# Kernel tuning notes

Hardware: AMD Instinct MI355X
Metric: run time of the kernel (lower is better)

## Reference

```python
import jax, jax.numpy as jnp
import numpy as np
import math

IN_FEATURES = 1024
OUT_FEATURES = 1024
N_BANK = 8192
N_LAYER = 12
N_EMBD = 1024


def setup_inputs() -> dict:
    key = jax.random.key(0)
    kq, kk, kv = jax.random.split(key, 3)
    q = jax.random.normal(kq, (4, 2048, IN_FEATURES), dtype=jnp.float32)
    k = 0.02 * jax.random.normal(kk, (N_BANK, IN_FEATURES), dtype=jnp.float32)
    v_std = 2.0 / N_LAYER / math.sqrt(N_EMBD)
    v = v_std * jax.random.normal(kv, (N_BANK, OUT_FEATURES), dtype=jnp.float32)
    return {"q": q, "k": k, "v": v}


def reference(q, k, v):
    # scores: [B, T, N]
    scores = jnp.einsum("btd,nd->btn", q, k)
    # row-wise L2 normalization, scaled by sqrt(N), then exact (erf) GELU
    sqrt_n = jnp.sqrt(jnp.asarray(scores.shape[-1], scores.dtype))
    norm = jnp.linalg.norm(scores, axis=-1, keepdims=True)
    gated = jax.nn.gelu(scores / norm * sqrt_n, approximate=False)
    # out: [B, T, out_features]
    return jnp.einsum("btn,no->bto", gated, v)
```

## Files before the change

### kernel.cpp

```cpp
#include <hip/hip_runtime.h>
#include <hip/hip_bf16.h>
#include <math.h>


#define MROWS 8192
#define DIN   1024
#define NBANK 8192
#define DOUT  1024

typedef float  f32x4  __attribute__((ext_vector_type(4)));
typedef __bf16 bf16x8 __attribute__((ext_vector_type(8)));

__device__ __forceinline__ float bf2f(unsigned short u) {
  union { unsigned int i; float f; } x; x.i = ((unsigned int)u) << 16; return x.f;
}
__device__ __forceinline__ unsigned short f2bf(float f) {
  union { float f; unsigned int i; } x; x.f = f;
  unsigned int u = x.i;
  unsigned int r = (u + 0x7fffu + ((u >> 16) & 1u)) >> 16;
  return (unsigned short)r;
}

__global__ void cvt_kernel(const float* __restrict__ src,
                           unsigned short* __restrict__ dst, int n) {
  int i = (blockIdx.x * 256 + threadIdx.x) * 4;
  if (i >= n) return;
  float4 vv = *(const float4*)(src + i);
  ushort4 o;
  o.x = f2bf(vv.x); o.y = f2bf(vv.y); o.z = f2bf(vv.z); o.w = f2bf(vv.w);
  *(ushort4*)(dst + i) = o;
}

__global__ void transpose_cvt_kernel(const float* __restrict__ src,
                                     unsigned short* __restrict__ dst,
                                     int R, int C) {
  __shared__ float tile[32][33];
  int c0 = blockIdx.x * 32, r0 = blockIdx.y * 32;
  for (int i = threadIdx.y; i < 32; i += 8)
    tile[i][threadIdx.x] = src[(size_t)(r0 + i) * C + c0 + threadIdx.x];
  __syncthreads();
  for (int i = threadIdx.y; i < 32; i += 8)
    dst[(size_t)(c0 + i) * R + r0 + threadIdx.x] = f2bf(tile[threadIdx.x][i]);
}

__global__ void zero_f32_kernel(float* __restrict__ p, int n4) {
  int i = blockIdx.x * 256 + threadIdx.x;
  if (i < n4) ((float4*)p)[i] = make_float4(0.f, 0.f, 0.f, 0.f);
}

__global__ __launch_bounds__(512, 4) void gemm1_kernel(
    const unsigned short* __restrict__ A, const unsigned short* __restrict__ B,
    unsigned short* __restrict__ C, float* __restrict__ sumsq) {
  __shared__ unsigned short As[3 * 4096];
  __shared__ unsigned short Bs[3 * 8192];
  const int K = DIN;
  const int NKT = DIN / 32;

  const int tid  = threadIdx.x;
  const int lane = tid & 63;
  const int wm   = (tid >> 6) >> 2;
  const int wn   = (tid >> 6) & 3;
  const int quad = lane >> 4;
  const int l16  = lane & 15;

  const int flat = blockIdx.y * gridDim.x + blockIdx.x;
  const int nwg  = gridDim.x * gridDim.y;
  const int swz  = (flat & 7) * (nwg >> 3) + (flat >> 3);
  const size_t m0 = (size_t)(swz / gridDim.x) * 128;
  const size_t n0 = (size_t)(swz % gridDim.x) * 256;

  const int sw   = (l16 >> 1) & 3;
  const int aoff = (wm * 64 + l16) * 32 + (quad ^ sw) * 8;
  const int boff = (wn * 64 + l16) * 32 + (quad ^ sw) * 8;

  const int gslot = (tid & 3) ^ ((tid >> 3) & 3);
  const unsigned short* Ag = A + (m0 + (tid >> 2)) * (size_t)K + gslot * 8;
  const unsigned short* Bg = B + (n0 + (tid >> 2)) * (size_t)K + gslot * 8;

  f32x4 acc[4][4];
#pragma unroll
  for (int i = 0; i < 4; i++)
#pragma unroll
    for (int j = 0; j < 4; j++) {
      f32x4 z = {0.f, 0.f, 0.f, 0.f};
      acc[i][j] = z;
    }

  auto stage = [&](int buf, int koff) {
    __builtin_amdgcn_global_load_lds(
        (const __attribute__((address_space(1))) unsigned int*)(Ag + koff),
        (__attribute__((address_space(3))) unsigned int*)(As + buf * 4096 + tid * 8),
        16, 0, 0);
    __builtin_amdgcn_global_load_lds(
        (const __attribute__((address_space(1))) unsigned int*)(Bg + koff),
        (__attribute__((address_space(3))) unsigned int*)(Bs + buf * 8192 + tid * 8),
        16, 0, 0);
    __builtin_amdgcn_global_load_lds(
        (const __attribute__((address_space(1))) unsigned int*)(Bg + (size_t)128 * K +
                                                                koff),
        (__attribute__((address_space(3))) unsigned int*)(Bs + buf * 8192 + 4096 +
                                                          tid * 8),
        16, 0, 0);
  };

  stage(0, 0);
  stage(1, 32);
  asm volatile("s_waitcnt vmcnt(3)" ::: "memory");
  __builtin_amdgcn_s_barrier();
  __builtin_amdgcn_sched_barrier(0);

  int cur = 0;
  for (int t = 0; t < NKT; ++t) {
    const bool pf = (t + 2) < NKT;
    if (pf) {
      int nxt = cur + 2;
      if (nxt >= 3) nxt -= 3;
      stage(nxt, (t + 2) * 32);
    }

    const unsigned short* Ab = As + cur * 4096 + aoff;
    const unsigned short* Bb = Bs + cur * 8192 + boff;
    bf16x8 a[4], b[4];
#pragma unroll
    for (int i = 0; i < 4; ++i) a[i] = *(const bf16x8*)(Ab + i * 512);
#pragma unroll
    for (int j = 0; j < 4; ++j) b[j] = *(const bf16x8*)(Bb + j * 512);

    asm volatile("s_waitcnt lgkmcnt(0)" ::: "memory");
    __builtin_amdgcn_sched_barrier(0);
    __builtin_amdgcn_s_setprio(1);
#pragma unroll
    for (int i = 0; i < 4; ++i)
#pragma unroll
      for (int j = 0; j < 4; ++j)
        acc[i][j] = __builtin_amdgcn_mfma_f32_16x16x32_bf16(a[i], b[j], acc[i][j],
                                                            0, 0, 0);
    __builtin_amdgcn_s_setprio(0);

    if (pf)
      asm volatile("s_waitcnt vmcnt(3)" ::: "memory");
    else
      asm volatile("s_waitcnt vmcnt(0)" ::: "memory");
    __builtin_amdgcn_s_barrier();
    __builtin_amdgcn_sched_barrier(0);

    cur = (cur == 2) ? 0 : cur + 1;
  }

#pragma unroll
  for (int mf = 0; mf < 4; ++mf)
#pragma unroll
    for (int r = 0; r < 4; ++r) {
      size_t row = m0 + wm * 64 + mf * 16 + quad * 4 + r;
      float s = 0.f;
#pragma unroll
      for (int nf = 0; nf < 4; ++nf) {
        float val = acc[mf][nf][r];
        s += val * val;
        C[row * (size_t)NBANK + n0 + wn * 64 + nf * 16 + l16] = f2bf(val);
      }
      s += __shfl_xor(s, 1);
      s += __shfl_xor(s, 2);
      s += __shfl_xor(s, 4);
      s += __shfl_xor(s, 8);
      if (l16 == 0) atomicAdd(&sumsq[row], s);
    }
}

__global__ void gelu_kernel(unsigned short* __restrict__ S,
                            const float* __restrict__ sumsq) {
  const size_t total = (size_t)MROWS * NBANK / 8;
  for (size_t u = (size_t)blockIdx.x * 256 + threadIdx.x; u < total;
       u += (size_t)gridDim.x * 256) {
    size_t idx = u * 8;
    int row = (int)(idx >> 13);
    float sc = sqrtf((float)NBANK / sumsq[row]);
    uint4 vv = *(const uint4*)(S + idx);
    unsigned int w[4] = {vv.x, vv.y, vv.z, vv.w};
#pragma unroll
    for (int e = 0; e < 4; e++) {
      float x0 = bf2f((unsigned short)(w[e] & 0xffffu)) * sc;
      float x1 = bf2f((unsigned short)(w[e] >> 16)) * sc;
      float g0 = 0.5f * x0 * (1.0f + erff(x0 * 0.70710678118654752f));
      float g1 = 0.5f * x1 * (1.0f + erff(x1 * 0.70710678118654752f));
      w[e] = (unsigned int)f2bf(g0) | ((unsigned int)f2bf(g1) << 16);
    }
    uint4 o; o.x = w[0]; o.y = w[1]; o.z = w[2]; o.w = w[3];
    *(uint4*)(S + idx) = o;
  }
}

__global__ __launch_bounds__(256, 4) void gemm2_kernel(
    const unsigned short* __restrict__ A,
    const unsigned short* __restrict__ B,
    float* __restrict__ C) {
  __shared__ unsigned short As[128 * 32];
  __shared__ unsigned short Bs[128 * 32];
  const int K = NBANK, ldc = DOUT;

  const int tid  = threadIdx.x;
  const int lane = tid & 63;
  const int wave = tid >> 6;
  const int wm   = (wave >> 1) * 64;
  const int wn   = (wave & 1) * 64;
  const int quad = lane >> 4;
  const int l16  = lane & 15;

  const int flat = blockIdx.y * gridDim.x + blockIdx.x;
  const int nwg  = gridDim.x * gridDim.y;
  const int swz  = (flat & 7) * (nwg >> 3) + (flat >> 3);
  const size_t m0 = (size_t)(swz / gridDim.x) * 128;
  const size_t n0 = (size_t)(swz % gridDim.x) * 128;

  const int srow = tid >> 2;
  const int scol = (((tid & 3) ^ ((tid >> 3) & 3))) * 8;
  const unsigned short* Ag0 = A + (m0 + srow) * (size_t)K + scol;
  const unsigned short* Ag1 = A + (m0 + srow + 64) * (size_t)K + scol;
  const unsigned short* Bg0 = B + (n0 + srow) * (size_t)K + scol;
  const unsigned short* Bg1 = B + (n0 + srow + 64) * (size_t)K + scol;

  unsigned short* AsW0 = As + tid * 8;
  unsigned short* AsW1 = As + 64 * 32 + tid * 8;
  unsigned short* BsW0 = Bs + tid * 8;
  unsigned short* BsW1 = Bs + 64 * 32 + tid * 8;

  const int sw = (l16 >> 1) & 3;
  const unsigned short* ArP = As + (wm + l16) * 32 + (quad ^ sw) * 8;
  const unsigned short* BrP = Bs + (wn + l16) * 32 + (quad ^ sw) * 8;

  f32x4 acc[4][4];
#pragma unroll
  for (int i = 0; i < 4; i++)
#pragma unroll
    for (int j = 0; j < 4; j++) {
      f32x4 z = {0.f, 0.f, 0.f, 0.f};
      acc[i][j] = z;
    }

  for (int k0 = 0; k0 < K; k0 += 32) {
    __builtin_amdgcn_global_load_lds(
        (const __attribute__((address_space(1))) unsigned int*)(Ag0 + k0),
        (__attribute__((address_space(3))) unsigned int*)AsW0, 16, 0, 0);
    __builtin_amdgcn_global_load_lds(
        (const __attribute__((address_space(1))) unsigned int*)(Ag1 + k0),
        (__attribute__((address_space(3))) unsigned int*)AsW1, 16, 0, 0);
    __builtin_amdgcn_global_load_lds(
        (const __attribute__((address_space(1))) unsigned int*)(Bg0 + k0),
        (__attribute__((address_space(3))) unsigned int*)BsW0, 16, 0, 0);
    __builtin_amdgcn_global_load_lds(
        (const __attribute__((address_space(1))) unsigned int*)(Bg1 + k0),
        (__attribute__((address_space(3))) unsigned int*)BsW1, 16, 0, 0);
    __syncthreads();

    bf16x8 af[4], bfr[4];
#pragma unroll
    for (int i = 0; i < 4; i++) af[i] = *(const bf16x8*)(ArP + i * 16 * 32);
#pragma unroll
    for (int j = 0; j < 4; j++) bfr[j] = *(const bf16x8*)(BrP + j * 16 * 32);
#pragma unroll
    for (int i = 0; i < 4; i++)
#pragma unroll
      for (int j = 0; j < 4; j++)
        acc[i][j] = __builtin_amdgcn_mfma_f32_16x16x32_bf16(af[i], bfr[j],
                                                            acc[i][j], 0, 0, 0);
    __syncthreads();
  }

#pragma unroll
  for (int i = 0; i < 4; i++)
#pragma unroll
    for (int j = 0; j < 4; j++)
#pragma unroll
      for (int r = 0; r < 4; r++) {
        size_t row = m0 + wm + i * 16 + quad * 4 + r;
        size_t col = n0 + wn + j * 16 + l16;
        C[row * (size_t)ldc + col] = acc[i][j][r];
      }
}

extern "C" void kernel_launch(void* const* d_in, const int* in_sizes, int n_in,
                              void* d_out, int out_size, void* d_ws, size_t ws_size,
                              hipStream_t stream) {
  const float* q = (const float*)d_in[0];
  const float* k = (const float*)d_in[1];
  const float* v = (const float*)d_in[2];
  float* out = (float*)d_out;

  char* ws = (char*)d_ws;
  const size_t MB = 1024ull * 1024ull;
  unsigned short* qb     = (unsigned short*)(ws);
  unsigned short* kb     = (unsigned short*)(ws + 16 * MB);
  unsigned short* vbT    = (unsigned short*)(ws + 32 * MB);
  unsigned short* scores = (unsigned short*)(ws + 48 * MB);
  float*          scale  = (float*)(ws + 176 * MB);

  const int nqk = MROWS * DIN;

  zero_f32_kernel<<<(MROWS / 4 + 255) / 256, 256, 0, stream>>>(scale, MROWS / 4);

  cvt_kernel<<<nqk / 1024, 256, 0, stream>>>(q, qb, nqk);
  cvt_kernel<<<nqk / 1024, 256, 0, stream>>>(k, kb, nqk);
  transpose_cvt_kernel<<<dim3(DOUT / 32, NBANK / 32), dim3(32, 8), 0, stream>>>(
      v, vbT, NBANK, DOUT);

  gemm1_kernel<<<dim3(NBANK / 256, MROWS / 128), 512, 0, stream>>>(qb, kb, scores,
                                                                   scale);

  gelu_kernel<<<4096, 256, 0, stream>>>(scores, scale);

  gemm2_kernel<<<dim3(DOUT / 128, MROWS / 128), 256, 0, stream>>>(scores, vbT, out);
}
```

Measured before the change: 551.0 us.

## Merge prep kernels, enlarge GEMM1 tile to 256x256, use sigmoid GELU approximation

Folds the zeroing, the two bf16 conversions and the V transpose into one prep kernel launch to cut launch overhead. GEMM1 moves from 128x256 to 256x256 tiles with 8x4 MFMA fragments per wave and drops the 3-stage LDS ring for plain double buffering, raising arithmetic intensity at the cost of more registers and a shallower prefetch. The exact erf GELU is replaced by a tanh-style sigmoid approximation using fast exp and rcp, which cuts transcendental cost but changes the numerics slightly.

New measurement: 1.673 ms. 204% more time.

```diff
diff --git a/kernel.cpp b/kernel.cpp
--- a/kernel.cpp
+++ b/kernel.cpp
@@ -21,38 +21,43 @@
   return (unsigned short)r;
 }
 
-__global__ void cvt_kernel(const float* __restrict__ src,
-                           unsigned short* __restrict__ dst, int n) {
-  int i = (blockIdx.x * 256 + threadIdx.x) * 4;
-  if (i >= n) return;
-  float4 vv = *(const float4*)(src + i);
-  ushort4 o;
-  o.x = f2bf(vv.x); o.y = f2bf(vv.y); o.z = f2bf(vv.z); o.w = f2bf(vv.w);
-  *(ushort4*)(dst + i) = o;
-}
-
-__global__ void transpose_cvt_kernel(const float* __restrict__ src,
-                                     unsigned short* __restrict__ dst,
-                                     int R, int C) {
+__global__ void prep_kernel(const float* __restrict__ q, const float* __restrict__ k,
+                            const float* __restrict__ v,
+                            unsigned short* __restrict__ qb,
+                            unsigned short* __restrict__ kb,
+                            unsigned short* __restrict__ vbT,
+                            float* __restrict__ sumsq) {
   __shared__ float tile[32][33];
-  int c0 = blockIdx.x * 32, r0 = blockIdx.y * 32;
-  for (int i = threadIdx.y; i < 32; i += 8)
-    tile[i][threadIdx.x] = src[(size_t)(r0 + i) * C + c0 + threadIdx.x];
-  __syncthreads();
-  for (int i = threadIdx.y; i < 32; i += 8)
-    dst[(size_t)(c0 + i) * R + r0 + threadIdx.x] = f2bf(tile[threadIdx.x][i]);
-}
-
-__global__ void zero_f32_kernel(float* __restrict__ p, int n4) {
-  int i = blockIdx.x * 256 + threadIdx.x;
-  if (i < n4) ((float4*)p)[i] = make_float4(0.f, 0.f, 0.f, 0.f);
+  const int b = blockIdx.x;
+  if (b < 16384) {
+    const float* src = (b < 8192) ? q : k;
+    unsigned short* dst = (b < 8192) ? qb : kb;
+    int i = ((b & 8191) * 256 + threadIdx.x) * 4;
+    float4 vv = *(const float4*)(src + i);
+    ushort4 o;
+    o.x = f2bf(vv.x); o.y = f2bf(vv.y); o.z = f2bf(vv.z); o.w = f2bf(vv.w);
+    *(ushort4*)(dst + i) = o;
+  } else if (b < 24576) {
+    int t = b - 16384;
+    int c0 = (t & 31) * 32;
+    int r0 = (t >> 5) * 32;
+    int tx = threadIdx.x & 31, ty = threadIdx.x >> 5;
+    for (int i = ty; i < 32; i += 8)
+      tile[i][tx] = v[(size_t)(r0 + i) * DOUT + c0 + tx];
+    __syncthreads();
+    for (int i = ty; i < 32; i += 8)
+      vbT[(size_t)(c0 + i) * NBANK + r0 + tx] = f2bf(tile[tx][i]);
+  } else {
+    int i = (b - 24576) * 256 + threadIdx.x;
+    ((float4*)sumsq)[i] = make_float4(0.f, 0.f, 0.f, 0.f);
+  }
 }
 
 __global__ __launch_bounds__(512, 4) void gemm1_kernel(
     const unsigned short* __restrict__ A, const unsigned short* __restrict__ B,
     unsigned short* __restrict__ C, float* __restrict__ sumsq) {
-  __shared__ unsigned short As[3 * 4096];
-  __shared__ unsigned short Bs[3 * 8192];
+  __shared__ unsigned short As[2 * 8192];
+  __shared__ unsigned short Bs[2 * 8192];
   const int K = DIN;
   const int NKT = DIN / 32;
 
@@ -66,22 +71,22 @@
   const int flat = blockIdx.y * gridDim.x + blockIdx.x;
   const int nwg  = gridDim.x * gridDim.y;
   const int swz  = (flat & 7) * (nwg >> 3) + (flat >> 3);
-  const size_t m0 = (size_t)(swz / gridDim.x) * 128;
+  const size_t m0 = (size_t)(swz / gridDim.x) * 256;
   const size_t n0 = (size_t)(swz % gridDim.x) * 256;
 
   const int sw   = (l16 >> 1) & 3;
-  const int aoff = (wm * 64 + l16) * 32 + (quad ^ sw) * 8;
+  const int aoff = (wm * 128 + l16) * 32 + (quad ^ sw) * 8;
   const int boff = (wn * 64 + l16) * 32 + (quad ^ sw) * 8;
 
   const int gslot = (tid & 3) ^ ((tid >> 3) & 3);
   const unsigned short* Ag = A + (m0 + (tid >> 2)) * (size_t)K + gslot * 8;
   const unsigned short* Bg = B + (n0 + (tid >> 2)) * (size_t)K + gslot * 8;
 
-  f32x4 acc[4][4];
-#pragma unroll
-  for (int i = 0; i < 4; i++)
-#pragma unroll
-    for (int j = 0; j < 4; j++) {
+  f32x4 acc[8][4];
+#pragma unroll
+  for (int i = 0; i < 8; ++i)
+#pragma unroll
+    for (int j = 0; j < 4; ++j) {
       f32x4 z = {0.f, 0.f, 0.f, 0.f};
       acc[i][j] = z;
     }
@@ -89,7 +94,13 @@
   auto stage = [&](int buf, int koff) {
     __builtin_amdgcn_global_load_lds(
         (const __attribute__((address_space(1))) unsigned int*)(Ag + koff),
-        (__attribute__((address_space(3))) unsigned int*)(As + buf * 4096 + tid * 8),
+        (__attribute__((address_space(3))) unsigned int*)(As + buf * 8192 + tid * 8),
+        16, 0, 0);
+    __builtin_amdgcn_global_load_lds(
+        (const __attribute__((address_space(1))) unsigned int*)(Ag + (size_t)128 * K +
+                                                                koff),
+        (__attribute__((address_space(3))) unsigned int*)(As + buf * 8192 + 4096 +
+                                                          tid * 8),
         16, 0, 0);
     __builtin_amdgcn_global_load_lds(
         (const __attribute__((address_space(1))) unsigned int*)(Bg + koff),
@@ -104,25 +115,18 @@
   };
 
   stage(0, 0);
-  stage(1, 32);
-  asm volatile("s_waitcnt vmcnt(3)" ::: "memory");
+  asm volatile("s_waitcnt vmcnt(0)" ::: "memory");
   __builtin_amdgcn_s_barrier();
-  __builtin_amdgcn_sched_barrier(0);
-
-  int cur = 0;
+
   for (int t = 0; t < NKT; ++t) {
-    const bool pf = (t + 2) < NKT;
-    if (pf) {
-      int nxt = cur + 2;
-      if (nxt >= 3) nxt -= 3;
-      stage(nxt, (t + 2) * 32);
-    }
-
-    const unsigned short* Ab = As + cur * 4096 + aoff;
+    const int cur = t & 1;
+    if (t + 1 < NKT) stage(cur ^ 1, (t + 1) * 32);
+
+    const unsigned short* Ab = As + cur * 8192 + aoff;
     const unsigned short* Bb = Bs + cur * 8192 + boff;
-    bf16x8 a[4], b[4];
-#pragma unroll
-    for (int i = 0; i < 4; ++i) a[i] = *(const bf16x8*)(Ab + i * 512);
+    bf16x8 a[8], b[4];
+#pragma unroll
+    for (int i = 0; i < 8; ++i) a[i] = *(const bf16x8*)(Ab + i * 512);
 #pragma unroll
     for (int j = 0; j < 4; ++j) b[j] = *(const bf16x8*)(Bb + j * 512);
 
@@ -130,28 +134,22 @@
     __builtin_amdgcn_sched_barrier(0);
     __builtin_amdgcn_s_setprio(1);
 #pragma unroll
-    for (int i = 0; i < 4; ++i)
+    for (int i = 0; i < 8; ++i)
 #pragma unroll
       for (int j = 0; j < 4; ++j)
         acc[i][j] = __builtin_amdgcn_mfma_f32_16x16x32_bf16(a[i], b[j], acc[i][j],
                                                             0, 0, 0);
     __builtin_amdgcn_s_setprio(0);
 
-    if (pf)
-      asm volatile("s_waitcnt vmcnt(3)" ::: "memory");
-    else
-      asm volatile("s_waitcnt vmcnt(0)" ::: "memory");
+    asm volatile("s_waitcnt vmcnt(0)" ::: "memory");
     __builtin_amdgcn_s_barrier();
-    __builtin_amdgcn_sched_barrier(0);
-
-    cur = (cur == 2) ? 0 : cur + 1;
   }
 
 #pragma unroll
-  for (int mf = 0; mf < 4; ++mf)
+  for (int mf = 0; mf < 8; ++mf)
 #pragma unroll
     for (int r = 0; r < 4; ++r) {
-      size_t row = m0 + wm * 64 + mf * 16 + quad * 4 + r;
+      size_t row = m0 + wm * 128 + mf * 16 + quad * 4 + r;
       float s = 0.f;
 #pragma unroll
       for (int nf = 0; nf < 4; ++nf) {
@@ -181,8 +179,10 @@
     for (int e = 0; e < 4; e++) {
       float x0 = bf2f((unsigned short)(w[e] & 0xffffu)) * sc;
       float x1 = bf2f((unsigned short)(w[e] >> 16)) * sc;
-      float g0 = 0.5f * x0 * (1.0f + erff(x0 * 0.70710678118654752f));
-      float g1 = 0.5f * x1 * (1.0f + erff(x1 * 0.70710678118654752f));
+      float t0 = x0 * (1.5957691f + 0.071354816f * x0 * x0);
+      float t1 = x1 * (1.5957691f + 0.071354816f * x1 * x1);
+      float g0 = x0 * __builtin_amdgcn_rcpf(1.f + __expf(-t0));
+      float g1 = x1 * __builtin_amdgcn_rcpf(1.f + __expf(-t1));
       w[e] = (unsigned int)f2bf(g0) | ((unsigned int)f2bf(g1) << 16);
     }
     uint4 o; o.x = w[0]; o.y = w[1]; o.z = w[2]; o.w = w[3];
@@ -294,16 +294,9 @@
   unsigned short* scores = (unsigned short*)(ws + 48 * MB);
   float*          scale  = (float*)(ws + 176 * MB);
 
-  const int nqk = MROWS * DIN;
-
-  zero_f32_kernel<<<(MROWS / 4 + 255) / 256, 256, 0, stream>>>(scale, MROWS / 4);
-
-  cvt_kernel<<<nqk / 1024, 256, 0, stream>>>(q, qb, nqk);
-  cvt_kernel<<<nqk / 1024, 256, 0, stream>>>(k, kb, nqk);
-  transpose_cvt_kernel<<<dim3(DOUT / 32, NBANK / 32), dim3(32, 8), 0, stream>>>(
-      v, vbT, NBANK, DOUT);
-
-  gemm1_kernel<<<dim3(NBANK / 256, MROWS / 128), 512, 0, stream>>>(qb, kb, scores,
+  prep_kernel<<<24584, 256, 0, stream>>>(q, k, v, qb, kb, vbT, scale);
+
+  gemm1_kernel<<<dim3(NBANK / 256, MROWS / 256), 512, 0, stream>>>(qb, kb, scores,
                                                                    scale);
 
   gelu_kernel<<<4096, 256, 0, stream>>>(scores, scale);
```
